# Performance work log

Hardware: AMD Instinct MI355X
Metric: run time of the kernel (lower is better)

The kernel has to match this reference:

```python
import jax, jax.numpy as jnp
import numpy as np

E, TOPK, HID, FFN = 8, 2, 1024, 2048  # experts, top_k, hidden K, intermediate N
B, S = 2, 1024


def setup_inputs() -> dict:
    key = jax.random.key(0)
    ks = jax.random.split(key, 7)
    return {
        "x": jax.random.normal(ks[0], (B, S, HID), jnp.float32),
        "router_weight": jax.random.normal(ks[1], (E, HID), jnp.float32) * 0.02,
        "router_bias": jax.random.normal(ks[2], (E,), jnp.float32) * 0.02,
        "w1": jax.random.normal(ks[3], (E, 2 * FFN, HID), jnp.float32) * 0.02,  # [E,2N,K] gate|up
        "w1_bias": jax.random.normal(ks[4], (E, 2 * FFN), jnp.float32) * 0.02,
        "w2": jax.random.normal(ks[5], (E, HID, FFN), jnp.float32) * 0.02,      # [E,K,N]
        "w2_bias": jax.random.normal(ks[6], (E, HID), jnp.float32) * 0.02,
        "top_k": TOPK,
    }


def reference(x, router_weight, router_bias, w1, w1_bias, w2, w2_bias, top_k):
    Bb, Ss, K = x.shape
    xf = x.reshape(-1, K)                                   # [M,K]
    M = xf.shape[0]
    Ne = w1.shape[0]
    # --- route_tokens: softmax over experts, then top-k (megablocks style) ---
    logits = xf @ router_weight.T + router_bias             # [M,E]
    probs = jax.nn.softmax(logits, axis=-1)
    topk_w, topk_ids = jax.lax.top_k(probs, top_k)          # [M,topk]
    # combine weights: scatter top-k probs into dense [M,E]
    comb = jnp.zeros((M, Ne), xf.dtype).at[jnp.arange(M)[:, None], topk_ids].add(topk_w)
    # --- fused experts (dense combine formulation, same math as grouped GEMM) ---
    gu = jnp.einsum('mk,enk->men', xf, w1) + w1_bias[None]  # [M,E,2N]
    Nf = gu.shape[-1] // 2
    gate, up = gu[..., :Nf], gu[..., Nf:]
    h = jax.nn.silu(gate) * up                              # silu_and_mul (SwiGLU)
    down = jnp.einsum('men,ekn->mek', h, w2) + w2_bias[None]  # [M,E,K]
    out = jnp.einsum('mek,me->mk', down, comb)              # weighted combine
    return out.reshape(Bb, Ss, K), topk_w
```

## Files before the change

### kernel.cpp

```cpp
#include <hip/hip_runtime.h>
#include <hip/hip_bf16.h>
#include <math.h>

#define E_    8
#define HID_  1024
#define FFN_  2048
#define M_    2048
#define NP_   (M_*2)

typedef __attribute__((ext_vector_type(8))) short bf16x8;
typedef __attribute__((ext_vector_type(8))) short short8v;
typedef __attribute__((ext_vector_type(4))) float f32x4;

typedef const __attribute__((address_space(1))) void GVOID;
typedef __attribute__((address_space(3))) void LVOID;

#define VMCNT4 asm volatile("s_waitcnt vmcnt(4)" ::: "memory")
#define VMCNT0 asm volatile("s_waitcnt vmcnt(0)" ::: "memory")

__device__ __forceinline__ short f2bf(float f) {
    union { __hip_bfloat16 b; short s; } u;
    u.b = __float2bfloat16(f);
    return u.s;
}

__global__ __launch_bounds__(256) void cvt_w1_kernel(
    const float* __restrict__ w1, __hip_bfloat16* __restrict__ w1bf)
{
    const float4* src = (const float4*)w1;
    short8v* dst = (short8v*)w1bf;
    size_t cbase = (size_t)blockIdx.x * 1024;

    float4 a[4], b[4];
#pragma unroll
    for (int u = 0; u < 4; ++u) {
        size_t c = cbase + u*256 + threadIdx.x;
        a[u] = src[2*c];
        b[u] = src[2*c + 1];
    }
#pragma unroll
    for (int u = 0; u < 4; ++u) {
        size_t c = cbase + u*256 + threadIdx.x;
        short8v o;
        o[0] = f2bf(a[u].x); o[1] = f2bf(a[u].y);
        o[2] = f2bf(a[u].z); o[3] = f2bf(a[u].w);
        o[4] = f2bf(b[u].x); o[5] = f2bf(b[u].y);
        o[6] = f2bf(b[u].z); o[7] = f2bf(b[u].w);
        dst[c] = o;
    }
}

__global__ __launch_bounds__(64) void router_kernel(
    const float* __restrict__ x, const float* __restrict__ rw,
    const float* __restrict__ rb, int* __restrict__ ids,
    float* __restrict__ wts, int* __restrict__ cnt,
    float* __restrict__ topk_out, __hip_bfloat16* __restrict__ xb)
{
    const int m    = blockIdx.x;
    const int lane = threadIdx.x;
    const float4* xm4 = (const float4*)(x + (size_t)m * HID_);

    float4 xv[4];
#pragma unroll
    for (int j = 0; j < 4; ++j) xv[j] = xm4[j*64 + lane];

    short4* xbr = (short4*)(xb + (size_t)m * HID_);
#pragma unroll
    for (int j = 0; j < 4; ++j) {
        short4 o;
        o.x = f2bf(xv[j].x); o.y = f2bf(xv[j].y);
        o.z = f2bf(xv[j].z); o.w = f2bf(xv[j].w);
        xbr[j*64 + lane] = o;
    }

    float lg[E_];
#pragma unroll
    for (int e = 0; e < E_; ++e) {
        const float4* we4 = (const float4*)(rw + e * HID_);
        float s = 0.f;
#pragma unroll
        for (int j = 0; j < 4; ++j) {
            float4 w = we4[j*64 + lane];
            s = fmaf(xv[j].x, w.x, s);
            s = fmaf(xv[j].y, w.y, s);
            s = fmaf(xv[j].z, w.z, s);
            s = fmaf(xv[j].w, w.w, s);
        }
        lg[e] = s;
    }
#pragma unroll
    for (int off = 32; off; off >>= 1)
#pragma unroll
        for (int e = 0; e < E_; ++e) lg[e] += __shfl_xor(lg[e], off);

    if (lane == 0) {
        float l2[E_], p[E_];
        float mx = -1e30f;
#pragma unroll
        for (int e = 0; e < E_; ++e) { l2[e] = lg[e] + rb[e]; mx = fmaxf(mx, l2[e]); }
        float sum = 0.f;
#pragma unroll
        for (int e = 0; e < E_; ++e) { p[e] = expf(l2[e] - mx); sum += p[e]; }
        float inv = 1.f / sum;
#pragma unroll
        for (int e = 0; e < E_; ++e) p[e] *= inv;

        int   i1 = -1, i2 = -1;
        float v1 = -1e30f, v2 = -1e30f;
#pragma unroll
        for (int e = 0; e < E_; ++e) {
            float pe = p[e];
            if (pe > v1)      { v2 = v1; i2 = i1; v1 = pe; i1 = e; }
            else if (pe > v2) { v2 = pe; i2 = e; }
        }
        ids[2*m]   = i1;  ids[2*m+1]   = i2;
        wts[2*m]   = v1;  wts[2*m+1]   = v2;
        topk_out[2*m]   = v1;
        topk_out[2*m+1] = v2;
        atomicAdd(&cnt[i1], 1);
        atomicAdd(&cnt[i2], 1);
    }
}

__global__ void offsets_kernel(const int* __restrict__ cnt,
                               int* __restrict__ off, int* __restrict__ fill)
{
    if (threadIdx.x == 0 && blockIdx.x == 0) {
        int acc = 0;
        for (int e = 0; e < E_; ++e) { off[e] = acc; fill[e] = acc; acc += cnt[e]; }
    }
}

__global__ __launch_bounds__(256) void scatter_kernel(
    const int* __restrict__ ids, const float* __restrict__ wts,
    int* __restrict__ fill, int* __restrict__ gtok, float* __restrict__ gwt,
    int* __restrict__ pos)
{
    int m = blockIdx.x * 256 + threadIdx.x;
    if (m >= M_) return;
#pragma unroll
    for (int s = 0; s < 2; ++s) {
        int e = ids[2*m + s];
        int p = atomicAdd(&fill[e], 1);
        gtok[p] = m;
        gwt[p]  = wts[2*m + s];
        pos[2*m + s] = p;
    }
}


__global__ __launch_bounds__(256, 3) void gemm1_kernel(
    const __hip_bfloat16* __restrict__ xb, const __hip_bfloat16* __restrict__ w1bf,
    const float* __restrict__ w1b, const int* __restrict__ gtok,
    const int* __restrict__ cnt, const int* __restrict__ off,
    __hip_bfloat16* __restrict__ h,
    const float* __restrict__ w2, __hip_bfloat16* __restrict__ w2bf)
{
    if (blockIdx.z == 8) {
        int pb = blockIdx.x + 32 * blockIdx.y;
        const float4* src = (const float4*)w2;
        short8v* dst = (short8v*)w2bf;
        size_t cb0 = (size_t)pb * 4096;
        for (int it = 0; it < 4; ++it) {
            size_t cbase = cb0 + it*1024;
            float4 a[4], b[4];
#pragma unroll
            for (int u = 0; u < 4; ++u) {
                size_t c = cbase + u*256 + threadIdx.x;
                a[u] = src[2*c];
                b[u] = src[2*c + 1];
            }
#pragma unroll
            for (int u = 0; u < 4; ++u) {
                size_t c = cbase + u*256 + threadIdx.x;
                short8v o;
                o[0] = f2bf(a[u].x); o[1] = f2bf(a[u].y);
                o[2] = f2bf(a[u].z); o[3] = f2bf(a[u].w);
                o[4] = f2bf(b[u].x); o[5] = f2bf(b[u].y);
                o[6] = f2bf(b[u].z); o[7] = f2bf(b[u].w);
                dst[c] = o;
            }
        }
        return;
    }

    const int e  = blockIdx.z;
    const int ce = cnt[e];
    const int t0 = blockIdx.y * 128;
    if (t0 >= ce) return;
    const int n0   = blockIdx.x * 64;
    const int base = off[e];
    const __hip_bfloat16* w1e = w1bf + (size_t)e * (2*FFN_) * HID_;

    __shared__ __align__(16) __hip_bfloat16 As[3][128*32];
    __shared__ __align__(16) __hip_bfloat16 Bs[3][128*32];

    const int tid  = threadIdx.x;
    const int lane = tid & 63;
    const int wid  = tid >> 6;
    const int wm   = wid >> 1;
    const int wn   = wid & 1;

    const __hip_bfloat16 *asrc[2], *bsrc[2];
#pragma unroll
    for (int q = 0; q < 2; ++q) {
        int slot = q*256 + tid;
        int r = slot >> 2, p = slot & 3;
        int c = p ^ ((r >> 1) & 3);
        int rr  = min(t0 + r, ce - 1);
        asrc[q] = xb + (size_t)gtok[base + rr] * HID_ + c*8;
        int q2 = r >> 5, s = r & 31;
        int grow = (q2 & 1) ? (FFN_ + n0 + (q2>>1)*32 + s)
                            : (       n0 + (q2>>1)*32 + s);
        bsrc[q] = w1e + (size_t)grow * HID_ + c*8;
    }

    auto STAGE = [&](int b, int k0) {
#pragma unroll
        for (int q = 0; q < 2; ++q)
            __builtin_amdgcn_global_load_lds((GVOID*)(asrc[q] + k0),
                (LVOID*)(&As[b][(q*256 + wid*64)*8]), 16, 0, 0);
#pragma unroll
        for (int q = 0; q < 2; ++q)
            __builtin_amdgcn_global_load_lds((GVOID*)(bsrc[q] + k0),
                (LVOID*)(&Bs[b][(q*256 + wid*64)*8]), 16, 0, 0);
    };

    f32x4 acc[4][4];
#pragma unroll
    for (int m = 0; m < 4; ++m)
#pragma unroll
        for (int n = 0; n < 4; ++n) acc[m][n] = (f32x4){0.f,0.f,0.f,0.f};

    const int cf = lane >> 4;
    auto COMPUTE = [&](int cb) {
        bf16x8 af[4], bfr[4];
#pragma unroll
        for (int m = 0; m < 4; ++m) {
            int r = wm*64 + m*16 + (lane & 15);
            int sw = cf ^ ((r >> 1) & 3);
            af[m] = *(bf16x8*)&As[cb][r*32 + sw*8];
        }
#pragma unroll
        for (int n = 0; n < 4; ++n) {
            int r = wn*64 + n*16 + (lane & 15);
            int sw = cf ^ ((r >> 1) & 3);
            bfr[n] = *(bf16x8*)&Bs[cb][r*32 + sw*8];
        }
        __builtin_amdgcn_s_setprio(1);
#pragma unroll
        for (int m = 0; m < 4; ++m)
#pragma unroll
            for (int n = 0; n < 4; ++n)
                acc[m][n] = __builtin_amdgcn_mfma_f32_16x16x32_bf16(
                    af[m], bfr[n], acc[m][n], 0, 0, 0);
        __builtin_amdgcn_s_setprio(0);
    };

    const int NT = HID_/32;
    STAGE(0, 0);
    STAGE(1, 32);
    VMCNT4;
    __builtin_amdgcn_s_barrier();

    int cb = 0;
    for (int t = 0; t < NT-2; ++t) {
        int sb = cb + 2; if (sb >= 3) sb -= 3;
        STAGE(sb, (t+2)*32);
        COMPUTE(cb);
        VMCNT4;
        __builtin_amdgcn_s_barrier();
        if (++cb == 3) cb = 0;
    }
    COMPUTE(cb);
    VMCNT0;
    __builtin_amdgcn_s_barrier();
    if (++cb == 3) cb = 0;
    COMPUTE(cb);

    const float* w1be = w1b + e*2*FFN_;
#pragma unroll
    for (int n = 0; n < 2; ++n) {
        int col = n0 + wn*32 + n*16 + (lane & 15);
        float bg = w1be[col];
        float bu = w1be[FFN_ + col];
#pragma unroll
        for (int m = 0; m < 4; ++m) {
            int rb2 = t0 + wm*64 + m*16 + (lane >> 4)*4;
#pragma unroll
            for (int i = 0; i < 4; ++i) {
                int t = rb2 + i;
                if (t < ce) {
                    float g = acc[m][n][i]   + bg;
                    float u = acc[m][n+2][i] + bu;
                    float hv = (g / (1.f + __expf(-g))) * u;
                    h[(size_t)(base + t)*FFN_ + col] = __float2bfloat16(hv);
                }
            }
        }
    }
}

__global__ __launch_bounds__(256, 3) void gemm2_kernel(
    const __hip_bfloat16* __restrict__ h, const __hip_bfloat16* __restrict__ w2bf,
    const float* __restrict__ w2b, const float* __restrict__ gwt,
    const int* __restrict__ cnt, const int* __restrict__ off,
    float* __restrict__ dpair)
{
    const int e  = blockIdx.z & 7;
    const int ks = blockIdx.z >> 3;
    const int ce = cnt[e];
    const int t0 = blockIdx.y * 128;
    if (t0 >= ce) return;
    const int n0    = blockIdx.x * 128;
    const int base  = off[e];
    const int kbase = ks * (FFN_/2);
    const __hip_bfloat16* w2e = w2bf + (size_t)e * HID_ * FFN_;

    __shared__ __align__(16) __hip_bfloat16 As[3][128*32];
    __shared__ __align__(16) __hip_bfloat16 Bs[3][128*32];

    const int tid  = threadIdx.x;
    const int lane = tid & 63;
    const int wid  = tid >> 6;
    const int wm   = wid >> 1;
    const int wn   = wid & 1;

    const __hip_bfloat16 *asrc[2], *bsrc[2];
#pragma unroll
    for (int q = 0; q < 2; ++q) {
        int slot = q*256 + tid;
        int r = slot >> 2, p = slot & 3;
        int c = p ^ ((r >> 1) & 3);
        int rr = min(t0 + r, ce - 1);
        asrc[q] = h   + (size_t)(base + rr) * FFN_ + kbase + c*8;
        bsrc[q] = w2e + (size_t)(n0 + r)    * FFN_ + kbase + c*8;
    }

    auto STAGE = [&](int b, int k0) {
#pragma unroll
        for (int q = 0; q < 2; ++q)
            __builtin_amdgcn_global_load_lds((GVOID*)(asrc[q] + k0),
                (LVOID*)(&As[b][(q*256 + wid*64)*8]), 16, 0, 0);
#pragma unroll
        for (int q = 0; q < 2; ++q)
            __builtin_amdgcn_global_load_lds((GVOID*)(bsrc[q] + k0),
                (LVOID*)(&Bs[b][(q*256 + wid*64)*8]), 16, 0, 0);
    };

    f32x4 acc[4][4];
#pragma unroll
    for (int m = 0; m < 4; ++m)
#pragma unroll
        for (int n = 0; n < 4; ++n) acc[m][n] = (f32x4){0.f,0.f,0.f,0.f};

    const int cf = lane >> 4;
    auto COMPUTE = [&](int cb) {
        bf16x8 af[4], bfr[4];
#pragma unroll
        for (int m = 0; m < 4; ++m) {
            int r = wm*64 + m*16 + (lane & 15);
            int sw = cf ^ ((r >> 1) & 3);
            af[m] = *(bf16x8*)&As[cb][r*32 + sw*8];
        }
#pragma unroll
        for (int n = 0; n < 4; ++n) {
            int r = wn*64 + n*16 + (lane & 15);
            int sw = cf ^ ((r >> 1) & 3);
            bfr[n] = *(bf16x8*)&Bs[cb][r*32 + sw*8];
        }
        __builtin_amdgcn_s_setprio(1);
#pragma unroll
        for (int m = 0; m < 4; ++m)
#pragma unroll
            for (int n = 0; n < 4; ++n)
                acc[m][n] = __builtin_amdgcn_mfma_f32_16x16x32_bf16(
                    af[m], bfr[n], acc[m][n], 0, 0, 0);
        __builtin_amdgcn_s_setprio(0);
    };

    const int NT = (FFN_/2)/32;
    STAGE(0, 0);
    STAGE(1, 32);
    VMCNT4;
    __builtin_amdgcn_s_barrier();

    int cb = 0;
    for (int t = 0; t < NT-2; ++t) {
        int sb = cb + 2; if (sb >= 3) sb -= 3;
        STAGE(sb, (t+2)*32);
        COMPUTE(cb);
        VMCNT4;
        __builtin_amdgcn_s_barrier();
        if (++cb == 3) cb = 0;
    }
    COMPUTE(cb);
    VMCNT0;
    __builtin_amdgcn_s_barrier();
    if (++cb == 3) cb = 0;
    COMPUTE(cb);

    const float* w2be = w2b + e*HID_;
    float* dpk = dpair + (size_t)ks * NP_ * HID_;
#pragma unroll
    for (int n = 0; n < 4; ++n) {
        int col = n0 + wn*64 + n*16 + (lane & 15);
        float bias = (ks == 0) ? w2be[col] : 0.f;
#pragma unroll
        for (int m = 0; m < 4; ++m) {
            int rb2 = t0 + wm*64 + m*16 + (lane >> 4)*4;
#pragma unroll
            for (int i = 0; i < 4; ++i) {
                int t = rb2 + i;
                if (t < ce) {
                    int p   = base + t;
                    float w = gwt[p];
                    dpk[(size_t)p*HID_ + col] = w * (acc[m][n][i] + bias);
                }
            }
        }
    }
}

__global__ __launch_bounds__(256) void combine_kernel(
    const float* __restrict__ dpair, const int* __restrict__ pos,
    float* __restrict__ out)
{
    int idx = blockIdx.x * 256 + threadIdx.x;
    int m   = idx >> 8;
    int c4  = (idx & 255) * 4;
    int p0 = pos[2*m], p1 = pos[2*m+1];
    const float* d0 = dpair;
    const float* d1 = dpair + (size_t)NP_ * HID_;
    float4 a0 = *(const float4*)(d0 + (size_t)p0*HID_ + c4);
    float4 a1 = *(const float4*)(d1 + (size_t)p0*HID_ + c4);
    float4 b0 = *(const float4*)(d0 + (size_t)p1*HID_ + c4);
    float4 b1 = *(const float4*)(d1 + (size_t)p1*HID_ + c4);
    float4 o = make_float4((a0.x+a1.x)+(b0.x+b1.x), (a0.y+a1.y)+(b0.y+b1.y),
                           (a0.z+a1.z)+(b0.z+b1.z), (a0.w+a1.w)+(b0.w+b1.w));
    *(float4*)(out + (size_t)m*HID_ + c4) = o;
}

__global__ __launch_bounds__(256) void gemm1_rs_kernel(
    const __hip_bfloat16* __restrict__ xb, const float* __restrict__ w1,
    const float* __restrict__ w1b, const int* __restrict__ gtok,
    const int* __restrict__ cnt, const int* __restrict__ off,
    __hip_bfloat16* __restrict__ h)
{
    const int e  = blockIdx.z;
    const int ce = cnt[e];
    const int t0 = blockIdx.y * 128;
    if (t0 >= ce) return;
    const int n0   = blockIdx.x * 64;
    const int base = off[e];
    const float* w1e = w1 + (size_t)e * (2*FFN_) * HID_;

    __shared__ __align__(16) __hip_bfloat16 As[128*64];
    __shared__ __align__(16) __hip_bfloat16 Bs[128*64];

    const int tid  = threadIdx.x;
    const int lane = tid & 63;
    const int wid  = tid >> 6;
    const int wm   = wid >> 1;
    const int wn   = wid & 1;

    const __hip_bfloat16* asrc[4];
#pragma unroll
    for (int q = 0; q < 4; ++q) {
        int slot = q*256 + tid;
        int r = slot >> 3, p = slot & 7;
        int rr  = min(t0 + r, ce - 1);
        int tok = gtok[base + rr];
        int c = p ^ (r & 7);
        asrc[q] = xb + (size_t)tok * HID_ + c*8;
    }

    const int brow = tid >> 1;
    const int hk   = tid & 1;
    const int q2 = brow >> 5, s = brow & 31;
    const int grow = (q2 & 1) ? (FFN_ + n0 + (q2>>1)*32 + s)
                              : (       n0 + (q2>>1)*32 + s);
    const float* bsrc = w1e + (size_t)grow * HID_ + hk*32;

    f32x4 acc[4][4];
#pragma unroll
    for (int m = 0; m < 4; ++m)
#pragma unroll
        for (int n = 0; n < 4; ++n) acc[m][n] = (f32x4){0.f,0.f,0.f,0.f};

    float4 breg[8];
#pragma unroll
    for (int j = 0; j < 8; ++j) breg[j] = *(const float4*)(bsrc + j*4);

    for (int k0 = 0; k0 < HID_; k0 += 64) {
#pragma unroll
        for (int q = 0; q < 4; ++q) {
            __builtin_amdgcn_global_load_lds(
                (GVOID*)(asrc[q] + k0),
                (LVOID*)(&As[(q*256 + wid*64)*8]), 16, 0, 0);
        }
#pragma unroll
        for (int cc = 0; cc < 4; ++cc) {
            union { bf16x8 v; short s8[8]; } u;
            const float* f0 = (const float*)&breg[2*cc];
#pragma unroll
            for (int j = 0; j < 8; ++j) u.s8[j] = f2bf(f0[j]);
            int c = hk*4 + cc, p = c ^ (brow & 7);
            *(bf16x8*)&Bs[brow*64 + p*8] = u.v;
        }
        __syncthreads();

        if (k0 + 64 < HID_) {
#pragma unroll
            for (int j = 0; j < 8; ++j) breg[j] = *(const float4*)(bsrc + (k0+64) + j*4);
        }

        bf16x8 af[4][2], bfr[4][2];
#pragma unroll
        for (int m = 0; m < 4; ++m)
#pragma unroll
            for (int kk = 0; kk < 2; ++kk) {
                int r = wm*64 + m*16 + (lane & 15);
                int c = kk*4 + (lane >> 4), p = c ^ (r & 7);
                af[m][kk] = *(bf16x8*)&As[r*64 + p*8];
            }
#pragma unroll
        for (int n = 0; n < 4; ++n)
#pragma unroll
            for (int kk = 0; kk < 2; ++kk) {
                int r = wn*64 + n*16 + (lane & 15);
                int c = kk*4 + (lane >> 4), p = c ^ (r & 7);
                bfr[n][kk] = *(bf16x8*)&Bs[r*64 + p*8];
            }
#pragma unroll
        for (int kk = 0; kk < 2; ++kk)
#pragma unroll
            for (int m = 0; m < 4; ++m)
#pragma unroll
                for (int n = 0; n < 4; ++n)
                    acc[m][n] = __builtin_amdgcn_mfma_f32_16x16x32_bf16(
                        af[m][kk], bfr[n][kk], acc[m][n], 0, 0, 0);
        __syncthreads();
    }

    const float* w1be = w1b + e*2*FFN_;
#pragma unroll
    for (int n = 0; n < 2; ++n) {
        int col = n0 + wn*32 + n*16 + (lane & 15);
        float bg = w1be[col];
        float bu = w1be[FFN_ + col];
#pragma unroll
        for (int m = 0; m < 4; ++m) {
            int rb2 = t0 + wm*64 + m*16 + (lane >> 4)*4;
#pragma unroll
            for (int i = 0; i < 4; ++i) {
                int t = rb2 + i;
                if (t < ce) {
                    float g = acc[m][n][i]   + bg;
                    float u = acc[m][n+2][i] + bu;
                    float hv = (g / (1.f + __expf(-g))) * u;
                    h[(size_t)(base + t)*FFN_ + col] = __float2bfloat16(hv);
                }
            }
        }
    }
}

__global__ __launch_bounds__(256) void gemm2_rs_kernel(
    const __hip_bfloat16* __restrict__ h, const float* __restrict__ w2,
    const float* __restrict__ w2b, const int* __restrict__ gtok,
    const float* __restrict__ gwt, const int* __restrict__ cnt,
    const int* __restrict__ off, float* __restrict__ out)
{
    const int e  = blockIdx.z;
    const int ce = cnt[e];
    const int t0 = blockIdx.y * 128;
    if (t0 >= ce) return;
    const int n0   = blockIdx.x * 128;
    const int base = off[e];
    const float* w2e = w2 + (size_t)e * HID_ * FFN_;

    __shared__ __align__(16) __hip_bfloat16 As[128*64];
    __shared__ __align__(16) __hip_bfloat16 Bs[128*64];

    const int tid  = threadIdx.x;
    const int lane = tid & 63;
    const int wid  = tid >> 6;
    const int wm   = wid >> 1;
    const int wn   = wid & 1;

    const __hip_bfloat16* asrc[4];
#pragma unroll
    for (int q = 0; q < 4; ++q) {
        int slot = q*256 + tid;
        int r = slot >> 3, p = slot & 7;
        int rr = min(t0 + r, ce - 1);
        int c = p ^ (r & 7);
        asrc[q] = h + (size_t)(base + rr) * FFN_ + c*8;
    }

    const int brow = tid >> 1;
    const int hk   = tid & 1;
    const float* bsrc = w2e + (size_t)(n0 + brow) * FFN_ + hk*32;

    f32x4 acc[4][4];
#pragma unroll
    for (int m = 0; m < 4; ++m)
#pragma unroll
        for (int n = 0; n < 4; ++n) acc[m][n] = (f32x4){0.f,0.f,0.f,0.f};

    float4 breg[8];
#pragma unroll
    for (int j = 0; j < 8; ++j) breg[j] = *(const float4*)(bsrc + j*4);

    for (int k0 = 0; k0 < FFN_; k0 += 64) {
#pragma unroll
        for (int q = 0; q < 4; ++q) {
            __builtin_amdgcn_global_load_lds(
                (GVOID*)(asrc[q] + k0),
                (LVOID*)(&As[(q*256 + wid*64)*8]), 16, 0, 0);
        }
#pragma unroll
        for (int cc = 0; cc < 4; ++cc) {
            union { bf16x8 v; short s8[8]; } u;
            const float* f0 = (const float*)&breg[2*cc];
#pragma unroll
            for (int j = 0; j < 8; ++j) u.s8[j] = f2bf(f0[j]);
            int c = hk*4 + cc, p = c ^ (brow & 7);
            *(bf16x8*)&Bs[brow*64 + p*8] = u.v;
        }
        __syncthreads();

        if (k0 + 64 < FFN_) {
#pragma unroll
            for (int j = 0; j < 8; ++j) breg[j] = *(const float4*)(bsrc + (k0+64) + j*4);
        }

        bf16x8 af[4][2], bfr[4][2];
#pragma unroll
        for (int m = 0; m < 4; ++m)
#pragma unroll
            for (int kk = 0; kk < 2; ++kk) {
                int r = wm*64 + m*16 + (lane & 15);
                int c = kk*4 + (lane >> 4), p = c ^ (r & 7);
                af[m][kk] = *(bf16x8*)&As[r*64 + p*8];
            }
#pragma unroll
        for (int n = 0; n < 4; ++n)
#pragma unroll
            for (int kk = 0; kk < 2; ++kk) {
                int r = wn*64 + n*16 + (lane & 15);
                int c = kk*4 + (lane >> 4), p = c ^ (r & 7);
                bfr[n][kk] = *(bf16x8*)&Bs[r*64 + p*8];
            }
#pragma unroll
        for (int kk = 0; kk < 2; ++kk)
#pragma unroll
            for (int m = 0; m < 4; ++m)
#pragma unroll
                for (int n = 0; n < 4; ++n)
                    acc[m][n] = __builtin_amdgcn_mfma_f32_16x16x32_bf16(
                        af[m][kk], bfr[n][kk], acc[m][n], 0, 0, 0);
        __syncthreads();
    }

    const float* w2be = w2b + e*HID_;
#pragma unroll
    for (int n = 0; n < 4; ++n) {
        int col = n0 + wn*64 + n*16 + (lane & 15);
        float bias = w2be[col];
#pragma unroll
        for (int m = 0; m < 4; ++m) {
            int rb2 = t0 + wm*64 + m*16 + (lane >> 4)*4;
#pragma unroll
            for (int i = 0; i < 4; ++i) {
                int t = rb2 + i;
                if (t < ce) {
                    int p   = base + t;
                    float w = gwt[p];
                    atomicAdd(&out[(size_t)gtok[p]*HID_ + col], w * (acc[m][n][i] + bias));
                }
            }
        }
    }
}

extern "C" void kernel_launch(void* const* d_in, const int* in_sizes, int n_in,
                              void* d_out, int out_size, void* d_ws, size_t ws_size,
                              hipStream_t stream)
{
    const float* x   = (const float*)d_in[0];
    const float* rw  = (const float*)d_in[1];
    const float* rb  = (const float*)d_in[2];
    const float* w1  = (const float*)d_in[3];
    const float* w1b = (const float*)d_in[4];
    const float* w2  = (const float*)d_in[5];
    const float* w2b = (const float*)d_in[6];

    float* out      = (float*)d_out;
    float* topk_out = out + (size_t)M_ * HID_;

    char*  ws   = (char*)d_ws;
    int*   ids  = (int*)  (ws);
    float* wts  = (float*)(ws + 16384);
    int*   gtok = (int*)  (ws + 32768);
    float* gwt  = (float*)(ws + 49152);
    int*   cnt  = (int*)  (ws + 65536);
    int*   off  = (int*)  (ws + 65536 + 128);
    int*   fill = (int*)  (ws + 65536 + 256);
    int*   pos  = (int*)  (ws + 98304);

    const size_t MB = 1024*1024;
    __hip_bfloat16* xb    = (__hip_bfloat16*)(ws + 131072);
    __hip_bfloat16* h     = (__hip_bfloat16*)(ws + 131072 + 4*MB);
    float*          dpair = (float*)         (ws + 131072 + 20*MB);
    __hip_bfloat16* w1bf  = (__hip_bfloat16*)(ws + 131072 + 52*MB);
    __hip_bfloat16* w2bf  = (__hip_bfloat16*)(ws + 131072 + 116*MB);
    const bool tier2 = (ws_size >= 131072 + 148*MB);

    hipMemsetAsync(cnt, 0, E_ * sizeof(int), stream);

    router_kernel<<<M_, 64, 0, stream>>>(x, rw, rb, ids, wts, cnt, topk_out, xb);
    offsets_kernel<<<1, 64, 0, stream>>>(cnt, off, fill);
    scatter_kernel<<<M_/256, 256, 0, stream>>>(ids, wts, fill, gtok, gwt, pos);

    if (tier2) {
        cvt_w1_kernel<<<4096, 256, 0, stream>>>(w1, w1bf);

        dim3 g1(FFN_/64, M_/128, E_ + 1);
        gemm1_kernel<<<g1, 256, 0, stream>>>(xb, w1bf, w1b, gtok, cnt, off, h,
                                             w2, w2bf);

        dim3 g2(HID_/128, M_/128, 2*E_);
        gemm2_kernel<<<g2, 256, 0, stream>>>(h, w2bf, w2b, gwt, cnt, off, dpair);

        combine_kernel<<<(M_*HID_)/(256*4), 256, 0, stream>>>(dpair, pos, out);
    } else {
        hipMemsetAsync(out, 0, (size_t)M_ * HID_ * sizeof(float), stream);

        dim3 g1(FFN_/64, M_/128, E_);
        gemm1_rs_kernel<<<g1, 256, 0, stream>>>(xb, w1, w1b, gtok, cnt, off, h);

        dim3 g2(HID_/128, M_/128, E_);
        gemm2_rs_kernel<<<g2, 256, 0, stream>>>(h, w2, w2b, gtok, gwt, cnt, off, out);
    }
}
```

Measured before the change: 237.7 us.

## Fuse w1 fp32-to-bf16 conversion into gemm1 LDS staging, drop cvt kernel

Removes the separate w1 conversion kernel. gemm1 now streams fp32 w1 tiles straight into LDS and packs them to bf16 with v_cvt_pk_bf16_f32 while loading MFMA fragments. The goal is to avoid writing and re-reading a 64MB bf16 copy of w1. In exchange, each gemm1 block reads twice the weight bytes per tile and re-reads fp32 weights across token tiles. Shared memory grows, so the pipeline is cut from triple to double buffering with full __syncthreads barriers, which could lower occupancy and overlap.

```diff
diff --git a/kernel.cpp b/kernel.cpp
--- a/kernel.cpp
+++ b/kernel.cpp
@@ -11,6 +11,7 @@
 typedef __attribute__((ext_vector_type(8))) short bf16x8;
 typedef __attribute__((ext_vector_type(8))) short short8v;
 typedef __attribute__((ext_vector_type(4))) float f32x4;
+typedef __attribute__((ext_vector_type(4))) int   i32x4;
 
 typedef const __attribute__((address_space(1))) void GVOID;
 typedef __attribute__((address_space(3))) void LVOID;
@@ -24,30 +25,15 @@
     return u.s;
 }
 
-__global__ __launch_bounds__(256) void cvt_w1_kernel(
-    const float* __restrict__ w1, __hip_bfloat16* __restrict__ w1bf)
-{
-    const float4* src = (const float4*)w1;
-    short8v* dst = (short8v*)w1bf;
-    size_t cbase = (size_t)blockIdx.x * 1024;
-
-    float4 a[4], b[4];
-#pragma unroll
-    for (int u = 0; u < 4; ++u) {
-        size_t c = cbase + u*256 + threadIdx.x;
-        a[u] = src[2*c];
-        b[u] = src[2*c + 1];
-    }
-#pragma unroll
-    for (int u = 0; u < 4; ++u) {
-        size_t c = cbase + u*256 + threadIdx.x;
-        short8v o;
-        o[0] = f2bf(a[u].x); o[1] = f2bf(a[u].y);
-        o[2] = f2bf(a[u].z); o[3] = f2bf(a[u].w);
-        o[4] = f2bf(b[u].x); o[5] = f2bf(b[u].y);
-        o[6] = f2bf(b[u].z); o[7] = f2bf(b[u].w);
-        dst[c] = o;
-    }
+__device__ __forceinline__ bf16x8 pk8(f32x4 lo, f32x4 hi) {
+    unsigned u0, u1, u2, u3;
+    asm("v_cvt_pk_bf16_f32 %0, %1, %2" : "=v"(u0) : "v"(lo.x), "v"(lo.y));
+    asm("v_cvt_pk_bf16_f32 %0, %1, %2" : "=v"(u1) : "v"(lo.z), "v"(lo.w));
+    asm("v_cvt_pk_bf16_f32 %0, %1, %2" : "=v"(u2) : "v"(hi.x), "v"(hi.y));
+    asm("v_cvt_pk_bf16_f32 %0, %1, %2" : "=v"(u3) : "v"(hi.z), "v"(hi.w));
+    union { i32x4 i; bf16x8 b; } r;
+    r.i = (i32x4){(int)u0, (int)u1, (int)u2, (int)u3};
+    return r.b;
 }
 
 __global__ __launch_bounds__(64) void router_kernel(
@@ -148,9 +134,8 @@
     }
 }
 
-
 __global__ __launch_bounds__(256, 3) void gemm1_kernel(
-    const __hip_bfloat16* __restrict__ xb, const __hip_bfloat16* __restrict__ w1bf,
+    const __hip_bfloat16* __restrict__ xb, const float* __restrict__ w1,
     const float* __restrict__ w1b, const int* __restrict__ gtok,
     const int* __restrict__ cnt, const int* __restrict__ off,
     __hip_bfloat16* __restrict__ h,
@@ -190,18 +175,19 @@
     if (t0 >= ce) return;
     const int n0   = blockIdx.x * 64;
     const int base = off[e];
-    const __hip_bfloat16* w1e = w1bf + (size_t)e * (2*FFN_) * HID_;
-
-    __shared__ __align__(16) __hip_bfloat16 As[3][128*32];
-    __shared__ __align__(16) __hip_bfloat16 Bs[3][128*32];
+    const float* w1e = w1 + (size_t)e * (2*FFN_) * HID_;
+
+    __shared__ __align__(16) __hip_bfloat16 As[2][128*32];
+    __shared__ __align__(16) float          Bsf[2][128*32];
 
     const int tid  = threadIdx.x;
     const int lane = tid & 63;
     const int wid  = tid >> 6;
     const int wm   = wid >> 1;
     const int wn   = wid & 1;
-
-    const __hip_bfloat16 *asrc[2], *bsrc[2];
+    const int cf   = lane >> 4;
+
+    const __hip_bfloat16* asrc[2];
 #pragma unroll
     for (int q = 0; q < 2; ++q) {
         int slot = q*256 + tid;
@@ -209,10 +195,17 @@
         int c = p ^ ((r >> 1) & 3);
         int rr  = min(t0 + r, ce - 1);
         asrc[q] = xb + (size_t)gtok[base + rr] * HID_ + c*8;
+    }
+    const float* bsrc[4];
+#pragma unroll
+    for (int q = 0; q < 4; ++q) {
+        int slot = q*256 + tid;
+        int r = slot >> 3, p = slot & 7;
+        int c = p ^ (r & 7);
         int q2 = r >> 5, s = r & 31;
         int grow = (q2 & 1) ? (FFN_ + n0 + (q2>>1)*32 + s)
                             : (       n0 + (q2>>1)*32 + s);
-        bsrc[q] = w1e + (size_t)grow * HID_ + c*8;
+        bsrc[q] = w1e + (size_t)grow * HID_ + c*4;
     }
 
     auto STAGE = [&](int b, int k0) {
@@ -221,9 +214,9 @@
             __builtin_amdgcn_global_load_lds((GVOID*)(asrc[q] + k0),
                 (LVOID*)(&As[b][(q*256 + wid*64)*8]), 16, 0, 0);
 #pragma unroll
-        for (int q = 0; q < 2; ++q)
+        for (int q = 0; q < 4; ++q)
             __builtin_amdgcn_global_load_lds((GVOID*)(bsrc[q] + k0),
-                (LVOID*)(&Bs[b][(q*256 + wid*64)*8]), 16, 0, 0);
+                (LVOID*)(&Bsf[b][(q*256 + wid*64)*4]), 16, 0, 0);
     };
 
     f32x4 acc[4][4];
@@ -232,7 +225,6 @@
 #pragma unroll
         for (int n = 0; n < 4; ++n) acc[m][n] = (f32x4){0.f,0.f,0.f,0.f};
 
-    const int cf = lane >> 4;
     auto COMPUTE = [&](int cb) {
         bf16x8 af[4], bfr[4];
 #pragma unroll
@@ -244,8 +236,11 @@
 #pragma unroll
         for (int n = 0; n < 4; ++n) {
             int r = wn*64 + n*16 + (lane & 15);
-            int sw = cf ^ ((r >> 1) & 3);
-            bfr[n] = *(bf16x8*)&Bs[cb][r*32 + sw*8];
+            int p0 = (2*cf)     ^ (r & 7);
+            int p1 = (2*cf + 1) ^ (r & 7);
+            f32x4 lo = *(f32x4*)&Bsf[cb][r*32 + p0*4];
+            f32x4 hi = *(f32x4*)&Bsf[cb][r*32 + p1*4];
+            bfr[n] = pk8(lo, hi);
         }
         __builtin_amdgcn_s_setprio(1);
 #pragma unroll
@@ -259,24 +254,13 @@
 
     const int NT = HID_/32;
     STAGE(0, 0);
-    STAGE(1, 32);
-    VMCNT4;
-    __builtin_amdgcn_s_barrier();
-
-    int cb = 0;
-    for (int t = 0; t < NT-2; ++t) {
-        int sb = cb + 2; if (sb >= 3) sb -= 3;
-        STAGE(sb, (t+2)*32);
-        COMPUTE(cb);
-        VMCNT4;
-        __builtin_amdgcn_s_barrier();
-        if (++cb == 3) cb = 0;
-    }
-    COMPUTE(cb);
-    VMCNT0;
-    __builtin_amdgcn_s_barrier();
-    if (++cb == 3) cb = 0;
-    COMPUTE(cb);
+    __syncthreads();
+    for (int t = 0; t < NT; ++t) {
+        int cur = t & 1, nxt = cur ^ 1;
+        if (t + 1 < NT) STAGE(nxt, (t+1)*32);
+        COMPUTE(cur);
+        __syncthreads();
+    }
 
     const float* w1be = w1b + e*2*FFN_;
 #pragma unroll
@@ -714,9 +698,8 @@
     __hip_bfloat16* xb    = (__hip_bfloat16*)(ws + 131072);
     __hip_bfloat16* h     = (__hip_bfloat16*)(ws + 131072 + 4*MB);
     float*          dpair = (float*)         (ws + 131072 + 20*MB);
-    __hip_bfloat16* w1bf  = (__hip_bfloat16*)(ws + 131072 + 52*MB);
-    __hip_bfloat16* w2bf  = (__hip_bfloat16*)(ws + 131072 + 116*MB);
-    const bool tier2 = (ws_size >= 131072 + 148*MB);
+    __hip_bfloat16* w2bf  = (__hip_bfloat16*)(ws + 131072 + 52*MB);
+    const bool tier2 = (ws_size >= 131072 + 84*MB);
 
     hipMemsetAsync(cnt, 0, E_ * sizeof(int), stream);
 
@@ -725,10 +708,8 @@
     scatter_kernel<<<M_/256, 256, 0, stream>>>(ids, wts, fill, gtok, gwt, pos);
 
     if (tier2) {
-        cvt_w1_kernel<<<4096, 256, 0, stream>>>(w1, w1bf);
-
         dim3 g1(FFN_/64, M_/128, E_ + 1);
-        gemm1_kernel<<<g1, 256, 0, stream>>>(xb, w1bf, w1b, gtok, cnt, off, h,
+        gemm1_kernel<<<g1, 256, 0, stream>>>(xb, w1, w1b, gtok, cnt, off, h,
                                              w2, w2bf);
 
         dim3 g2(HID_/128, M_/128, 2*E_);
```

After: 229.4 us. 1.04x faster.
